# Performance work log

Hardware: AMD Instinct MI355X
Metric: run time of the kernel (lower is better)

Reference implementation:

```python
import jax, jax.numpy as jnp
import numpy as np

B, S, D, H = 2, 2048, 1024, 16
DK = D // H


def setup_inputs() -> dict:
    key = jax.random.key(0)
    ks = jax.random.split(key, 12)
    sc = 1.0 / np.sqrt(D)
    inp = {
        "q": jax.random.normal(ks[0], (B, S, D), jnp.float32),
        "k": jax.random.normal(ks[1], (B, S, D), jnp.float32),
        "v": jax.random.normal(ks[2], (B, S, D), jnp.float32),
        "attn_mask": jnp.tril(jnp.ones((S, S), jnp.int32))[None, None],  # causal [1,1,S,S]
        "Wq": jax.random.normal(ks[3], (D, D), jnp.float32) * sc,
        "bq": jnp.zeros((D,), jnp.float32),
        "Wk": jax.random.normal(ks[4], (D, D), jnp.float32) * sc,
        "bk": jnp.zeros((D,), jnp.float32),
        "Wv": jax.random.normal(ks[5], (D, D), jnp.float32) * sc,
        "bv": jnp.zeros((D,), jnp.float32),
        "Wo": jax.random.normal(ks[6], (D, D), jnp.float32) * sc,
        "bo": jnp.zeros((D,), jnp.float32),
    }
    return inp


def reference(q, k, v, attn_mask, Wq, bq, Wk, bk, Wv, bv, Wo, bo):
    # projections: x @ W^T + b, then split heads -> [B,H,S,DK]
    def proj(x, W, b):
        y = jnp.einsum("bsd,ed->bse", x, W) + b
        return y.reshape(B, S, H, DK).transpose(0, 2, 1, 3)

    qh, kh, vh = proj(q, Wq, bq), proj(k, Wk, bk), proj(v, Wv, bv)
    scores = jnp.einsum("bhqd,bhkd->bhqk", qh, kh) / jnp.sqrt(jnp.float32(DK))
    scores = jnp.where(attn_mask == 0, jnp.float32(-1e9), scores)
    attn = jax.nn.softmax(scores, axis=-1)  # dropout p=0.0 -> identity
    ctx = jnp.einsum("bhqk,bhkd->bhqd", attn, vh)
    concat = ctx.transpose(0, 2, 1, 3).reshape(B, S, D)
    output = jnp.einsum("bsd,ed->bse", concat, Wo) + bo
    return output, attn
```

## Files before the change

### kernel.cpp

```cpp
#include <hip/hip_runtime.h>
#include <hip/hip_bf16.h>
#include <cstdint>
#include <cstddef>

#define DEV_INLINE __device__ __forceinline__

typedef float  f32x4  __attribute__((ext_vector_type(4)));
typedef __bf16 bf16x8 __attribute__((ext_vector_type(8)));
typedef __bf16 bf16x4 __attribute__((ext_vector_type(4)));

static constexpr int kB = 2, kS = 2048, kD = 1024, kH = 16, kDK = 64;
static constexpr int kM  = kB * kS;
static constexpr int kNX = kM * kD;
static constexpr int kNW = kD * kD;

DEV_INLINE void gld16(void* lds, const void* g) {
  __builtin_amdgcn_global_load_lds(
      (const __attribute__((address_space(1))) unsigned int*)g,
      (__attribute__((address_space(3))) unsigned int*)lds, 16, 0, 0);
}

__global__ __launch_bounds__(256) void cvt_kernel(
    const float* __restrict__ q, const float* __restrict__ k, const float* __restrict__ v,
    const float* __restrict__ wq, const float* __restrict__ wk, const float* __restrict__ wv,
    const float* __restrict__ wo, __bf16* __restrict__ xb, __bf16* __restrict__ wb) {
  const int z = blockIdx.y;
  const float* src;
  __bf16* dst;
  int n;
  switch (z) {
    case 0:  src = q;  dst = xb;           n = kNX; break;
    case 1:  src = k;  dst = xb + kNX;     n = kNX; break;
    case 2:  src = v;  dst = xb + 2 * kNX; n = kNX; break;
    case 3:  src = wq; dst = wb;           n = kNW; break;
    case 4:  src = wk; dst = wb + kNW;     n = kNW; break;
    case 5:  src = wv; dst = wb + 2 * kNW; n = kNW; break;
    default: src = wo; dst = wb + 3 * kNW; n = kNW; break;
  }
  const int i = (blockIdx.x * 256 + threadIdx.x) * 4;
  if (i < n) {
    float4 f = *(const float4*)(src + i);
    bf16x4 o;
    o[0] = (__bf16)f.x; o[1] = (__bf16)f.y; o[2] = (__bf16)f.z; o[3] = (__bf16)f.w;
    *(bf16x4*)(dst + i) = o;
  }
}

template <int MODE>
DEV_INLINE void gemm_core(__bf16* As, __bf16* Bs,
                          const __bf16* __restrict__ A, const __bf16* __restrict__ W,
                          const float* __restrict__ bias, void* __restrict__ dstv) {
  const int tid = threadIdx.x;
  const int w = tid >> 6, l = tid & 63;
  const int m0 = blockIdx.y * 128, n0 = blockIdx.x * 128;
  const int wr = (w >> 1) * 64, wc = (w & 1) * 64;
  const int fr = l & 15, fc = l >> 4;
  const int srow = tid >> 2;
  const int scol = (tid & 3) * 8;

  f32x4 acc[4][4];
  const f32x4 z4 = {0.f, 0.f, 0.f, 0.f};
#pragma unroll
  for (int mi = 0; mi < 4; ++mi)
#pragma unroll
    for (int ni = 0; ni < 4; ++ni) acc[mi][ni] = z4;

  for (int k0 = 0; k0 < kD; k0 += 32) {
    __syncthreads();
    gld16(As + (size_t)(w * 64) * 8,       A + (size_t)(m0 + srow) * kD + k0 + scol);
    gld16(As + (size_t)(256 + w * 64) * 8, A + (size_t)(m0 + 64 + srow) * kD + k0 + scol);
    gld16(Bs + (size_t)(w * 64) * 8,       W + (size_t)(n0 + srow) * kD + k0 + scol);
    gld16(Bs + (size_t)(256 + w * 64) * 8, W + (size_t)(n0 + 64 + srow) * kD + k0 + scol);
    __syncthreads();
    bf16x8 af[4], bfr[4];
#pragma unroll
    for (int mi = 0; mi < 4; ++mi)
      af[mi] = *(const bf16x8*)(As + (wr + mi * 16 + fr) * 32 + fc * 8);
#pragma unroll
    for (int ni = 0; ni < 4; ++ni)
      bfr[ni] = *(const bf16x8*)(Bs + (wc + ni * 16 + fr) * 32 + fc * 8);
#pragma unroll
    for (int mi = 0; mi < 4; ++mi)
#pragma unroll
      for (int ni = 0; ni < 4; ++ni)
        acc[mi][ni] = __builtin_amdgcn_mfma_f32_16x16x32_bf16(af[mi], bfr[ni], acc[mi][ni], 0, 0, 0);
  }

#pragma unroll
  for (int mi = 0; mi < 4; ++mi) {
#pragma unroll
    for (int ni = 0; ni < 4; ++ni) {
      const int col = n0 + wc + ni * 16 + fr;
      const float bb = bias[col];
#pragma unroll
      for (int r = 0; r < 4; ++r) {
        const int row = m0 + wr + mi * 16 + fc * 4 + r;
        const float val = acc[mi][ni][r] + bb;
        if (MODE == 2) {
          ((float*)dstv)[(size_t)row * kD + col] = val;
        } else {
          const int b = row >> 11, s = row & (kS - 1);
          const int h = col >> 6, dk = col & 63;
          size_t idx;
          if (MODE == 0) idx = ((size_t)(b * kH + h) * kS + s) * kDK + dk;
          else           idx = ((size_t)(b * kH + h) * kDK + dk) * kS + s;
          ((__bf16*)dstv)[idx] = (__bf16)val;
        }
      }
    }
  }
}

__global__ __launch_bounds__(256) void proj_kernel(
    const __bf16* __restrict__ xb, const __bf16* __restrict__ wb,
    const float* __restrict__ bq, const float* __restrict__ bk, const float* __restrict__ bv,
    __bf16* __restrict__ Qh, __bf16* __restrict__ Kh, __bf16* __restrict__ Vt) {
  __shared__ __attribute__((aligned(16))) __bf16 As[128 * 32];
  __shared__ __attribute__((aligned(16))) __bf16 Bs[128 * 32];
  const int z = blockIdx.z;
  const __bf16* A = xb + (size_t)z * kNX;
  const __bf16* W = wb + (size_t)z * kNW;
  if (z == 0)      gemm_core<0>(As, Bs, A, W, bq, Qh);
  else if (z == 1) gemm_core<0>(As, Bs, A, W, bk, Kh);
  else             gemm_core<1>(As, Bs, A, W, bv, Vt);
}

__global__ __launch_bounds__(256) void outproj_kernel(
    const __bf16* __restrict__ ctxb, const __bf16* __restrict__ wo,
    const float* __restrict__ bo, float* __restrict__ out) {
  __shared__ __attribute__((aligned(16))) __bf16 As[128 * 32];
  __shared__ __attribute__((aligned(16))) __bf16 Bs[128 * 32];
  gemm_core<2>(As, Bs, ctxb, wo, bo, out);
}

DEV_INLINE void qk_tile(const __bf16* __restrict__ Kh, size_t ktile_base,
                        bf16x8 aq0, bf16x8 aq1, int fr, int fc, f32x4 sc[4]) {
  const f32x4 z4 = {0.f, 0.f, 0.f, 0.f};
#pragma unroll
  for (int ni = 0; ni < 4; ++ni) sc[ni] = z4;
#pragma unroll
  for (int kc = 0; kc < 2; ++kc) {
    bf16x8 aq = kc ? aq1 : aq0;
#pragma unroll
    for (int ni = 0; ni < 4; ++ni) {
      bf16x8 bk = *(const bf16x8*)(Kh + ktile_base + (size_t)(ni * 16 + fr) * kDK + kc * 32 + fc * 8);
      sc[ni] = __builtin_amdgcn_mfma_f32_16x16x32_bf16(aq, bk, sc[ni], 0, 0, 0);
    }
  }
}

__global__ __launch_bounds__(256) void attn_kernel(
    const __bf16* __restrict__ Qh, const __bf16* __restrict__ Kh,
    const __bf16* __restrict__ Vt, float* __restrict__ attnp,
    __bf16* __restrict__ ctxb) {
  __shared__ __attribute__((aligned(16))) __bf16 Plds[4][16][72];
  const int qt = blockIdx.x, bh = blockIdx.y;
  const int tid = threadIdx.x, w = tid >> 6, l = tid & 63;
  const int fr = l & 15, fc = l >> 4;
  const int q0 = qt * 64;
  const int rowg = q0 + w * 16;
  const int nkt = qt + 1;

  const __bf16* qptr = Qh + ((size_t)bh * kS + rowg + fr) * kDK + fc * 8;
  const bf16x8 aq0 = *(const bf16x8*)(qptr);
  const bf16x8 aq1 = *(const bf16x8*)(qptr + 32);

  float mrow[4], lrow[4];
#pragma unroll
  for (int r = 0; r < 4; ++r) { mrow[r] = -1.0e30f; lrow[r] = 0.f; }

  for (int kt = 0; kt < nkt; ++kt) {
    f32x4 sc[4];
    qk_tile(Kh, ((size_t)bh * kS + kt * 64) * kDK, aq0, aq1, fr, fc, sc);
#pragma unroll
    for (int ni = 0; ni < 4; ++ni) {
      const int colg = kt * 64 + ni * 16 + fr;
#pragma unroll
      for (int r = 0; r < 4; ++r) {
        float s = sc[ni][r] * 0.125f;
        if (kt == qt && colg > rowg + fc * 4 + r) s = -1.0e30f;
        sc[ni][r] = s;
      }
    }
    float tmax[4];
#pragma unroll
    for (int r = 0; r < 4; ++r)
      tmax[r] = fmaxf(fmaxf(sc[0][r], sc[1][r]), fmaxf(sc[2][r], sc[3][r]));
#pragma unroll
    for (int off = 1; off < 16; off <<= 1)
#pragma unroll
      for (int r = 0; r < 4; ++r)
        tmax[r] = fmaxf(tmax[r], __shfl_xor(tmax[r], off));
#pragma unroll
    for (int r = 0; r < 4; ++r) {
      const float nm = fmaxf(mrow[r], tmax[r]);
      float ts = __expf(sc[0][r] - nm) + __expf(sc[1][r] - nm) +
                 __expf(sc[2][r] - nm) + __expf(sc[3][r] - nm);
#pragma unroll
      for (int off = 1; off < 16; off <<= 1) ts += __shfl_xor(ts, off);
      lrow[r] = lrow[r] * __expf(mrow[r] - nm) + ts;
      mrow[r] = nm;
    }
  }

  float invl[4];
#pragma unroll
  for (int r = 0; r < 4; ++r) invl[r] = 1.0f / lrow[r];

  f32x4 oacc[4];
  const f32x4 z4v = {0.f, 0.f, 0.f, 0.f};
#pragma unroll
  for (int ni = 0; ni < 4; ++ni) oacc[ni] = z4v;

  for (int kt = 0; kt < nkt; ++kt) {
    f32x4 sc[4];
    qk_tile(Kh, ((size_t)bh * kS + kt * 64) * kDK, aq0, aq1, fr, fc, sc);
#pragma unroll
    for (int ni = 0; ni < 4; ++ni) {
      const int colg = kt * 64 + ni * 16 + fr;
#pragma unroll
      for (int r = 0; r < 4; ++r) {
        float s = sc[ni][r] * 0.125f;
        if (kt == qt && colg > rowg + fc * 4 + r) s = -1.0e30f;
        const float p = __expf(s - mrow[r]) * invl[r];
        attnp[((size_t)bh * kS + rowg + fc * 4 + r) * kS + colg] = p;
        Plds[w][fc * 4 + r][ni * 16 + fr] = (__bf16)p;
      }
    }
#pragma unroll
    for (int kc = 0; kc < 2; ++kc) {
      bf16x8 ap = *(const bf16x8*)(&Plds[w][fr][kc * 32 + fc * 8]);
#pragma unroll
      for (int ni = 0; ni < 4; ++ni) {
        bf16x8 bv = *(const bf16x8*)(Vt + ((size_t)bh * kDK + ni * 16 + fr) * kS +
                                     kt * 64 + kc * 32 + fc * 8);
        oacc[ni] = __builtin_amdgcn_mfma_f32_16x16x32_bf16(ap, bv, oacc[ni], 0, 0, 0);
      }
    }
  }

  const int b = bh >> 4, h = bh & 15;
#pragma unroll
  for (int ni = 0; ni < 4; ++ni) {
#pragma unroll
    for (int r = 0; r < 4; ++r) {
      const int srow = rowg + fc * 4 + r;
      ctxb[((size_t)b * kS + srow) * kD + h * kDK + ni * 16 + fr] = (__bf16)oacc[ni][r];
    }
  }

  const int c0 = nkt * 64;
  const int zrow = tid >> 2;
  const int part = tid & 3;
  float* rowp = attnp + ((size_t)bh * kS + q0 + zrow) * kS;
  const float4 zf4 = {0.f, 0.f, 0.f, 0.f};
  for (int c = c0 + part * 4; c < kS; c += 16)
    *(float4*)(rowp + c) = zf4;
}

extern "C" void kernel_launch(void* const* d_in, const int* in_sizes, int n_in,
                              void* d_out, int out_size, void* d_ws, size_t ws_size,
                              hipStream_t stream) {
  (void)in_sizes; (void)n_in; (void)out_size; (void)ws_size;
  const float* q  = (const float*)d_in[0];
  const float* k  = (const float*)d_in[1];
  const float* v  = (const float*)d_in[2];
  const float* Wq = (const float*)d_in[4];
  const float* bq = (const float*)d_in[5];
  const float* Wk = (const float*)d_in[6];
  const float* bk = (const float*)d_in[7];
  const float* Wv = (const float*)d_in[8];
  const float* bv = (const float*)d_in[9];
  const float* Wo = (const float*)d_in[10];
  const float* bo = (const float*)d_in[11];

  float* out = (float*)d_out;
  float* attnp = out + (size_t)kNX;

  char* ws = (char*)d_ws;
  __bf16* xb = (__bf16*)ws;
  __bf16* wb = (__bf16*)(ws + (size_t)3 * kNX * 2);
  __bf16* Qh = (__bf16*)(ws + (size_t)3 * kNX * 2 + (size_t)4 * kNW * 2);
  __bf16* Kh = Qh + (size_t)kNX;
  __bf16* Vt = Kh + (size_t)kNX;
  __bf16* ctxb = xb;

  cvt_kernel<<<dim3(4096, 7), 256, 0, stream>>>(q, k, v, Wq, Wk, Wv, Wo, xb, wb);
  proj_kernel<<<dim3(8, 32, 3), 256, 0, stream>>>(xb, wb, bq, bk, bv, Qh, Kh, Vt);
  attn_kernel<<<dim3(32, 32), 256, 0, stream>>>(Qh, Kh, Vt, attnp, ctxb);
  outproj_kernel<<<dim3(8, 32), 256, 0, stream>>>(ctxb, wb + (size_t)3 * kNW, bo, out);
}
```

Measured before the change: 963.9 us.

## Pair causal query tiles per block, write V row-major then transpose separately

```diff
diff --git a/kernel.cpp b/kernel.cpp
--- a/kernel.cpp
+++ b/kernel.cpp
@@ -101,10 +101,7 @@
         } else {
           const int b = row >> 11, s = row & (kS - 1);
           const int h = col >> 6, dk = col & 63;
-          size_t idx;
-          if (MODE == 0) idx = ((size_t)(b * kH + h) * kS + s) * kDK + dk;
-          else           idx = ((size_t)(b * kH + h) * kDK + dk) * kS + s;
-          ((__bf16*)dstv)[idx] = (__bf16)val;
+          ((__bf16*)dstv)[((size_t)(b * kH + h) * kS + s) * kDK + dk] = (__bf16)val;
         }
       }
     }
@@ -114,7 +111,7 @@
 __global__ __launch_bounds__(256) void proj_kernel(
     const __bf16* __restrict__ xb, const __bf16* __restrict__ wb,
     const float* __restrict__ bq, const float* __restrict__ bk, const float* __restrict__ bv,
-    __bf16* __restrict__ Qh, __bf16* __restrict__ Kh, __bf16* __restrict__ Vt) {
+    __bf16* __restrict__ Qh, __bf16* __restrict__ Kh, __bf16* __restrict__ Vh) {
   __shared__ __attribute__((aligned(16))) __bf16 As[128 * 32];
   __shared__ __attribute__((aligned(16))) __bf16 Bs[128 * 32];
   const int z = blockIdx.z;
@@ -122,7 +119,30 @@
   const __bf16* W = wb + (size_t)z * kNW;
   if (z == 0)      gemm_core<0>(As, Bs, A, W, bq, Qh);
   else if (z == 1) gemm_core<0>(As, Bs, A, W, bk, Kh);
-  else             gemm_core<1>(As, Bs, A, W, bv, Vt);
+  else             gemm_core<0>(As, Bs, A, W, bv, Vh);
+}
+
+__global__ __launch_bounds__(256) void vtrans_kernel(
+    const __bf16* __restrict__ Vh, __bf16* __restrict__ Vt) {
+  __shared__ __bf16 T[64][65];
+  const int bh = blockIdx.y, st = blockIdx.x;
+  const int t = threadIdx.x;
+  const int r = t >> 3, c8 = (t & 7) * 8;
+  const size_t base = (size_t)bh * kS * kDK;
+#pragma unroll
+  for (int rr = 0; rr < 64; rr += 32) {
+    bf16x8 v = *(const bf16x8*)(Vh + base + (size_t)(st * 64 + r + rr) * kDK + c8);
+#pragma unroll
+    for (int j = 0; j < 8; ++j) T[r + rr][c8 + j] = v[j];
+  }
+  __syncthreads();
+#pragma unroll
+  for (int rr = 0; rr < 64; rr += 32) {
+    bf16x8 o;
+#pragma unroll
+    for (int j = 0; j < 8; ++j) o[j] = T[c8 + j][r + rr];
+    *(bf16x8*)(Vt + base + (size_t)(r + rr) * kS + st * 64 + c8) = o;
+  }
 }
 
 __global__ __launch_bounds__(256) void outproj_kernel(
@@ -149,19 +169,21 @@
   }
 }
 
-__global__ __launch_bounds__(256) void attn_kernel(
+__global__ __launch_bounds__(512, 4) void attn_kernel(
     const __bf16* __restrict__ Qh, const __bf16* __restrict__ Kh,
     const __bf16* __restrict__ Vt, float* __restrict__ attnp,
     __bf16* __restrict__ ctxb) {
-  __shared__ __attribute__((aligned(16))) __bf16 Plds[4][16][72];
-  const int qt = blockIdx.x, bh = blockIdx.y;
+  __shared__ __attribute__((aligned(16))) __bf16 Plds[8][16][72];
+  const int pair = blockIdx.x, bh = blockIdx.y;
   const int tid = threadIdx.x, w = tid >> 6, l = tid & 63;
+  const int wg = w >> 2, wi = w & 3;
+  const int qt = wg ? (31 - pair) : pair;
+  const int q0 = qt * 64;
+  const int rowg = q0 + wi * 16;
   const int fr = l & 15, fc = l >> 4;
-  const int q0 = qt * 64;
-  const int rowg = q0 + w * 16;
-  const int nkt = qt + 1;
-
-  const __bf16* qptr = Qh + ((size_t)bh * kS + rowg + fr) * kDK + fc * 8;
+  const size_t kbase = (size_t)bh * kS * kDK;
+
+  const __bf16* qptr = Qh + (kbase + (size_t)(rowg + fr) * kDK) + fc * 8;
   const bf16x8 aq0 = *(const bf16x8*)(qptr);
   const bf16x8 aq1 = *(const bf16x8*)(qptr + 32);
 
@@ -169,9 +191,41 @@
 #pragma unroll
   for (int r = 0; r < 4; ++r) { mrow[r] = -1.0e30f; lrow[r] = 0.f; }
 
-  for (int kt = 0; kt < nkt; ++kt) {
+  int kt = 0;
+  for (; kt + 2 <= qt; kt += 2) {
+    f32x4 s0[4], s1[4];
+    qk_tile(Kh, kbase + (size_t)kt * 64 * kDK, aq0, aq1, fr, fc, s0);
+    qk_tile(Kh, kbase + (size_t)(kt + 1) * 64 * kDK, aq0, aq1, fr, fc, s1);
+#pragma unroll
+    for (int ni = 0; ni < 4; ++ni)
+#pragma unroll
+      for (int r = 0; r < 4; ++r) { s0[ni][r] *= 0.125f; s1[ni][r] *= 0.125f; }
+    float tmax[4];
+#pragma unroll
+    for (int r = 0; r < 4; ++r)
+      tmax[r] = fmaxf(fmaxf(fmaxf(s0[0][r], s0[1][r]), fmaxf(s0[2][r], s0[3][r])),
+                      fmaxf(fmaxf(s1[0][r], s1[1][r]), fmaxf(s1[2][r], s1[3][r])));
+#pragma unroll
+    for (int off = 1; off < 16; off <<= 1)
+#pragma unroll
+      for (int r = 0; r < 4; ++r)
+        tmax[r] = fmaxf(tmax[r], __shfl_xor(tmax[r], off));
+#pragma unroll
+    for (int r = 0; r < 4; ++r) {
+      const float nm = fmaxf(mrow[r], tmax[r]);
+      float ts = __expf(s0[0][r] - nm) + __expf(s0[1][r] - nm) +
+                 __expf(s0[2][r] - nm) + __expf(s0[3][r] - nm) +
+                 __expf(s1[0][r] - nm) + __expf(s1[1][r] - nm) +
+                 __expf(s1[2][r] - nm) + __expf(s1[3][r] - nm);
+#pragma unroll
+      for (int off = 1; off < 16; off <<= 1) ts += __shfl_xor(ts, off);
+      lrow[r] = lrow[r] * __expf(mrow[r] - nm) + ts;
+      mrow[r] = nm;
+    }
+  }
+  for (; kt <= qt; ++kt) {
     f32x4 sc[4];
-    qk_tile(Kh, ((size_t)bh * kS + kt * 64) * kDK, aq0, aq1, fr, fc, sc);
+    qk_tile(Kh, kbase + (size_t)kt * 64 * kDK, aq0, aq1, fr, fc, sc);
 #pragma unroll
     for (int ni = 0; ni < 4; ++ni) {
       const int colg = kt * 64 + ni * 16 + fr;
@@ -212,17 +266,15 @@
 #pragma unroll
   for (int ni = 0; ni < 4; ++ni) oacc[ni] = z4v;
 
-  for (int kt = 0; kt < nkt; ++kt) {
-    f32x4 sc[4];
-    qk_tile(Kh, ((size_t)bh * kS + kt * 64) * kDK, aq0, aq1, fr, fc, sc);
+  auto pv_tile = [&](f32x4 sc[4], int kt2, bool masked) {
 #pragma unroll
     for (int ni = 0; ni < 4; ++ni) {
-      const int colg = kt * 64 + ni * 16 + fr;
+      const int colg = kt2 * 64 + ni * 16 + fr;
 #pragma unroll
       for (int r = 0; r < 4; ++r) {
-        float s = sc[ni][r] * 0.125f;
-        if (kt == qt && colg > rowg + fc * 4 + r) s = -1.0e30f;
-        const float p = __expf(s - mrow[r]) * invl[r];
+        float p;
+        if (masked && colg > rowg + fc * 4 + r) p = 0.f;
+        else p = __expf(sc[ni][r] * 0.125f - mrow[r]) * invl[r];
         attnp[((size_t)bh * kS + rowg + fc * 4 + r) * kS + colg] = p;
         Plds[w][fc * 4 + r][ni * 16 + fr] = (__bf16)p;
       }
@@ -232,11 +284,25 @@
       bf16x8 ap = *(const bf16x8*)(&Plds[w][fr][kc * 32 + fc * 8]);
 #pragma unroll
       for (int ni = 0; ni < 4; ++ni) {
-        bf16x8 bv = *(const bf16x8*)(Vt + ((size_t)bh * kDK + ni * 16 + fr) * kS +
-                                     kt * 64 + kc * 32 + fc * 8);
+        bf16x8 bv = *(const bf16x8*)(Vt + kbase + (size_t)(ni * 16 + fr) * kS +
+                                     kt2 * 64 + kc * 32 + fc * 8);
         oacc[ni] = __builtin_amdgcn_mfma_f32_16x16x32_bf16(ap, bv, oacc[ni], 0, 0, 0);
       }
     }
+  };
+
+  kt = 0;
+  for (; kt + 2 <= qt; kt += 2) {
+    f32x4 s0[4], s1[4];
+    qk_tile(Kh, kbase + (size_t)kt * 64 * kDK, aq0, aq1, fr, fc, s0);
+    qk_tile(Kh, kbase + (size_t)(kt + 1) * 64 * kDK, aq0, aq1, fr, fc, s1);
+    pv_tile(s0, kt, false);
+    pv_tile(s1, kt + 1, false);
+  }
+  for (; kt <= qt; ++kt) {
+    f32x4 sc[4];
+    qk_tile(Kh, kbase + (size_t)kt * 64 * kDK, aq0, aq1, fr, fc, sc);
+    pv_tile(sc, kt, kt == qt);
   }
 
   const int b = bh >> 4, h = bh & 15;
@@ -249,10 +315,9 @@
     }
   }
 
-  const int c0 = nkt * 64;
-  const int zrow = tid >> 2;
-  const int part = tid & 3;
-  float* rowp = attnp + ((size_t)bh * kS + q0 + zrow) * kS;
+  const int c0 = (qt + 1) * 64;
+  const int zr = l >> 2, part = l & 3;
+  float* rowp = attnp + ((size_t)bh * kS + rowg + zr) * kS;
   const float4 zf4 = {0.f, 0.f, 0.f, 0.f};
   for (int c = c0 + part * 4; c < kS; c += 16)
     *(float4*)(rowp + c) = zf4;
@@ -284,9 +349,11 @@
   __bf16* Kh = Qh + (size_t)kNX;
   __bf16* Vt = Kh + (size_t)kNX;
   __bf16* ctxb = xb;
+  __bf16* Vh = (__bf16*)attnp;
 
   cvt_kernel<<<dim3(4096, 7), 256, 0, stream>>>(q, k, v, Wq, Wk, Wv, Wo, xb, wb);
-  proj_kernel<<<dim3(8, 32, 3), 256, 0, stream>>>(xb, wb, bq, bk, bv, Qh, Kh, Vt);
-  attn_kernel<<<dim3(32, 32), 256, 0, stream>>>(Qh, Kh, Vt, attnp, ctxb);
+  proj_kernel<<<dim3(8, 32, 3), 256, 0, stream>>>(xb, wb, bq, bk, bv, Qh, Kh, Vh);
+  vtrans_kernel<<<dim3(32, 32), 256, 0, stream>>>(Vh, Vt);
+  attn_kernel<<<dim3(16, 32), 512, 0, stream>>>(Qh, Kh, Vt, attnp, ctxb);
   outproj_kernel<<<dim3(8, 32), 256, 0, stream>>>(ctxb, wb + (size_t)3 * kNW, bo, out);
 }
```

Result: faster. 896.7 us (-7.0%).
